# Performance work log

Hardware: AMD Instinct MI355X
Metric: run time of the kernel (lower is better)

The kernel has to match this reference:

```python
import jax, jax.numpy as jnp
import numpy as np
from jax import lax

V, E, H, T = 100000, 256, 256, 8192
FL, FN, NC = 5, 128, 20


def setup_inputs() -> dict:
    key = jax.random.key(0)
    ks = jax.random.split(key, 12)
    s = 0.05
    return {
        "docs": jax.random.randint(ks[0], (1, T), 0, V),
        "docs_length": jnp.array([T]),
        "labels": jax.random.randint(ks[1], (1,), 0, NC),
        "iteration": 0,
        "embed_W": jax.random.uniform(ks[2], (V, E), jnp.float32, -0.1, 0.1),
        "w_ih": jax.random.normal(ks[3], (4 * H, E), jnp.float32) * s,
        "w_hh": jax.random.normal(ks[4], (4 * H, H), jnp.float32) * s,
        "b_ih": jax.random.normal(ks[5], (4 * H,), jnp.float32) * s,
        "b_hh": jax.random.normal(ks[6], (4 * H,), jnp.float32) * s,
        "conv_w": jax.random.normal(ks[7], (FN, 1, FL, H), jnp.float32) * s,
        "conv_b": jax.random.normal(ks[8], (FN,), jnp.float32) * s,
        "logits_w": jax.random.uniform(ks[9], (NC, FN), jnp.float32, -0.1, 0.1),
        "logits_b": jnp.zeros((NC,), jnp.float32),
    }


def _forward(docs, labels, embed_W, w_ih, w_hh, b_ih, b_hh, conv_w, conv_b, logits_w, logits_b):
    # embed -> ReLU (dropout is identity at p=0)
    x = jax.nn.relu(embed_W[docs[0]])  # (T, E)

    b = b_ih + b_hh

    def step(carry, xt):
        h, c = carry
        g = xt @ w_ih.T + h @ w_hh.T + b  # (4H,)
        i, f, gg, o = jnp.split(g, 4)
        i = jax.nn.sigmoid(i)
        f = jax.nn.sigmoid(f)
        gg = jnp.tanh(gg)
        o = jax.nn.sigmoid(o)
        c = f * c + i * gg
        h = o * jnp.tanh(c)
        return (h, c), h

    init = (jnp.zeros((H,), x.dtype), jnp.zeros((H,), x.dtype))
    _, hs = lax.scan(step, init, x)  # (T, H)

    # Conv2d(1, FN, (FL, H)) valid: (1,1,T,H) -> (1,FN,T-FL+1,1)
    feat = lax.conv_general_dilated(
        hs[None, None, :, :], conv_w, window_strides=(1, 1), padding="VALID",
        dimension_numbers=("NCHW", "OIHW", "NCHW"))
    feat = feat[0, :, :, 0] + conv_b[:, None]  # (FN, T-FL+1)

    # AdaptiveMaxPool2d((FN,1)) == max over time
    pooled = jnp.max(feat, axis=1)  # (FN,)

    logits = pooled @ logits_w.T + logits_b  # (NC,)
    logp = jax.nn.log_softmax(logits)
    loss = -logp[labels[0]]
    acc = (jnp.argmax(logp) == labels[0]).astype(jnp.float32)
    return loss, acc


def reference(docs, docs_length, labels, iteration, embed_W, w_ih, w_hh, b_ih, b_hh,
              conv_w, conv_b, logits_w, logits_b):
    return _forward(docs, labels, embed_W, w_ih, w_hh, b_ih, b_hh,
                    conv_w, conv_b, logits_w, logits_b)
```

## Files before the change

### kernel.cpp

```cpp
#include <hip/hip_runtime.h>
#include <math.h>

#define T_LEN 8192

typedef float f32x4 __attribute__((ext_vector_type(4)));
typedef int   i32x8 __attribute__((ext_vector_type(8)));

#define DPP_MAX(x, ctrl) fmaxf((x), __int_as_float(__builtin_amdgcn_update_dpp(0, __float_as_int(x), (ctrl), 0xF, 0xF, true)))

__device__ __forceinline__ float fsig(float x) {
    x = fminf(30.f, fmaxf(-30.f, x));
    float e = __expf(-x);
    return __builtin_amdgcn_rcpf(1.f + e);
}
__device__ __forceinline__ float ftanh(float x) {
    x = fminf(15.f, fmaxf(-15.f, x));
    float e = __expf(-2.f * x);
    return (1.f - e) * __builtin_amdgcn_rcpf(1.f + e);
}

__device__ __forceinline__ unsigned char enc_e4m3(float x) {
#if __has_builtin(__builtin_amdgcn_cvt_pk_fp8_f32)
    int v = __builtin_amdgcn_cvt_pk_fp8_f32(x, 0.f, 0, false);
    return (unsigned char)(v & 0xff);
#else
    unsigned u = __float_as_uint(x);
    unsigned s = (u >> 24) & 0x80u;
    float a = fabsf(x);
    if (a > 448.f) a = 448.f;
    if (a < 9.765625e-4f) return (unsigned char)s;
    int e = ((int)((__float_as_uint(a) >> 23) & 0xffu)) - 127;
    int eu = e < -6 ? -6 : e;
    float ulp = exp2f((float)(eu - 3));
    float q = rintf(a / ulp);
    int mant, ee;
    if (eu == -6 && q < 8.f) { mant = (int)q; ee = 0; }
    else {
        if (q >= 16.f) { q *= 0.5f; eu += 1; }
        mant = (int)q - 8; ee = eu + 7;
        if (ee > 15 || (ee == 15 && mant > 6)) { ee = 15; mant = 6; }
    }
    return (unsigned char)(s | (unsigned)(ee << 3) | (unsigned)mant);
#endif
}
__device__ __forceinline__ unsigned pk4(float a, float b, float c, float d) {
    return (unsigned)enc_e4m3(a) | ((unsigned)enc_e4m3(b) << 8)
         | ((unsigned)enc_e4m3(c) << 16) | ((unsigned)enc_e4m3(d) << 24);
}

__device__ __forceinline__ unsigned enc_e2m3(float x) {
    unsigned s = (__float_as_uint(x) >> 31) << 5;
    float a = fabsf(x);
    a = fminf(a, 7.5f);
    if (a < 0.0625f) return s;
    int e = ((int)((__float_as_uint(a) >> 23) & 0xffu)) - 127;
    int eu = e < 0 ? 0 : e;
    float ulp = __int_as_float((unsigned)(eu + 124) << 23);
    float q = rintf(a * __builtin_amdgcn_rcpf(ulp));
    int E, M;
    if (e < 0) {
        if (q >= 8.f) { E = 1; M = 0; }
        else { E = 0; M = (int)q; }
    } else {
        if (q >= 16.f) { q = 8.f; eu += 1; }
        if (eu > 2) { E = 3; M = 7; }
        else { E = eu + 1; M = (int)q - 8; }
    }
    return s | (unsigned)(E << 3) | (unsigned)M;
}

__global__ __launch_bounds__(256) void pack_w6(
    const float* __restrict__ w_hh,
    unsigned* __restrict__ w6)
{
    int idx = blockIdx.x * 256 + threadIdx.x;
    int l  = idx & 63;
    int kt = (idx >> 6) & 1;
    int rt = (idx >> 7) & 7;
    int w  = idx >> 10;
    int rw = l & 15, kg = l >> 4;
    int rowp = ((8 * w + rt) << 4) + rw;
    int orow = ((rowp & 3) << 8) + (rowp >> 2);
    const float* s = w_hh + (size_t)orow * 256 + 128 * kt + 32 * kg;
    unsigned d[6] = {0, 0, 0, 0, 0, 0};
#pragma unroll
    for (int j = 0; j < 32; ++j) {
        unsigned c = enc_e2m3(s[j] * 32.f);
        int bit = 6 * j;
        d[bit >> 5] |= c << (bit & 31);
        if ((bit & 31) > 26) d[(bit >> 5) + 1] |= c >> (32 - (bit & 31));
    }
    unsigned* o = w6 + (size_t)idx * 8;
    o[0] = d[0]; o[1] = d[1]; o[2] = d[2];
    o[3] = d[3]; o[4] = d[4]; o[5] = d[5];
    o[6] = 0;    o[7] = 0;
}

__global__ __launch_bounds__(256, 4) void gemm_pre(
    const int* __restrict__ docs,
    const float* __restrict__ embW,
    const float* __restrict__ w_ih,
    const float* __restrict__ b_ih,
    const float* __restrict__ b_hh,
    float* __restrict__ pre)
{
    __shared__ __align__(16) float As[16][68];
    __shared__ __align__(16) float Bs[16][68];
    __shared__ int rowid[64];
    const int bt = blockIdx.x;
    const int bj = blockIdx.y;
    const int tid = threadIdx.x;
    if (tid < 64) rowid[tid] = docs[bt * 64 + tid];
    __syncthreads();
    const int ti = tid & 15, tj = tid >> 4;
    const int r = tid & 63;
    const int kk4 = (tid >> 6) * 4;
    float acc[4][4];
#pragma unroll
    for (int ii = 0; ii < 4; ++ii)
#pragma unroll
        for (int jj = 0; jj < 4; ++jj) acc[ii][jj] = 0.f;

    for (int k0 = 0; k0 < 256; k0 += 16) {
        float4 av = *(const float4*)(embW + (size_t)rowid[r] * 256 + k0 + kk4);
        float4 bv = *(const float4*)(w_ih + (size_t)(bj * 64 + r) * 256 + k0 + kk4);
        As[kk4 + 0][r] = fmaxf(av.x, 0.f);
        As[kk4 + 1][r] = fmaxf(av.y, 0.f);
        As[kk4 + 2][r] = fmaxf(av.z, 0.f);
        As[kk4 + 3][r] = fmaxf(av.w, 0.f);
        Bs[kk4 + 0][r] = bv.x;
        Bs[kk4 + 1][r] = bv.y;
        Bs[kk4 + 2][r] = bv.z;
        Bs[kk4 + 3][r] = bv.w;
        __syncthreads();
#pragma unroll
        for (int kk = 0; kk < 16; ++kk) {
            float4 a = *(const float4*)&As[kk][ti * 4];
            float4 b = *(const float4*)&Bs[kk][tj * 4];
            acc[0][0] += a.x * b.x; acc[0][1] += a.x * b.y; acc[0][2] += a.x * b.z; acc[0][3] += a.x * b.w;
            acc[1][0] += a.y * b.x; acc[1][1] += a.y * b.y; acc[1][2] += a.y * b.z; acc[1][3] += a.y * b.w;
            acc[2][0] += a.z * b.x; acc[2][1] += a.z * b.y; acc[2][2] += a.z * b.z; acc[2][3] += a.z * b.w;
            acc[3][0] += a.w * b.x; acc[3][1] += a.w * b.y; acc[3][2] += a.w * b.z; acc[3][3] += a.w * b.w;
        }
        __syncthreads();
    }
#pragma unroll
    for (int ii = 0; ii < 4; ++ii) {
        int t = bt * 64 + ti * 4 + ii;
#pragma unroll
        for (int jj = 0; jj < 4; ++jj) {
            int j = bj * 64 + tj * 4 + jj;
            int jp = ((j & 255) << 2) | (j >> 8);
            pre[(size_t)t * 1024 + jp] = acc[ii][jj] + b_ih[j] + b_hh[j];
        }
    }
}

__global__ __launch_bounds__(512, 2) void lstm_scan_mx6(
    const float* __restrict__ pre,
    const unsigned* __restrict__ w6,
    float* __restrict__ hs)
{
    const int tid = threadIdx.x;
    const int w  = tid >> 6;
    const int l  = tid & 63;
    const int rw = l & 15;
    const int kg = l >> 4;
    const float INV = 1.f / 128.f;

    __shared__ __align__(16) unsigned char h6pk[2][256];
    __shared__ __align__(16) float ldsPre[2][1024];

    i32x8 wA[8][2];
#pragma unroll
    for (int rt = 0; rt < 8; ++rt) {
#pragma unroll
        for (int kt = 0; kt < 2; ++kt) {
            const unsigned* s = w6 + (size_t)(((w * 8 + rt) * 2 + kt) * 64 + l) * 8;
            uint4 lo = *(const uint4*)s;
            uint2 hi = *(const uint2*)(s + 4);
            i32x8 v;
            v[0] = (int)lo.x; v[1] = (int)lo.y; v[2] = (int)lo.z;
            v[3] = (int)lo.w; v[4] = (int)hi.x; v[5] = (int)hi.y;
            v[6] = 0; v[7] = 0;
            wA[rt][kt] = v;
        }
    }

    for (int i = tid; i < 512; i += 512) h6pk[0][i] = 0;
    {
        float2 p = *(const float2*)(pre + 2 * tid);
        *(float2*)&ldsPre[0][2 * tid] = p;
    }

    const bool isup = (rw < 8);
    const int u = 32 * w + 4 * (rw & 7) + kg;
    float c_st = 0.f;

    const bool iswr = (rw < 8) && (kg < 3);
    const int bby = 8 * kg + rw;
    const int j0  = (4 * bby) / 3;
    const int rsh = 8 * bby - 6 * j0;
    const int lj0 = 16 * (j0 & 3) + (j0 >> 2);
    const int j1  = j0 + 1;
    const int lj1 = 16 * (j1 & 3) + (j1 >> 2);

    const float* pnext = pre + 1024 + 2 * tid;
    float* hsp = hs + u;
    __syncthreads();

    for (int t = 0; t < T_LEN; ++t) {
        const int PW = t & 1;
        const int PR = PW ^ 1;

        f32x4 p4 = *(const f32x4*)&ldsPre[PW][4 * u];

        float2 pv = *(const float2*)pnext;
        if (t + 2 < T_LEN) pnext += 1024;

        i32x8 bq[2];
#pragma unroll
        for (int kt = 0; kt < 2; ++kt) {
            const unsigned char* bp = &h6pk[PR][(4 * kt + kg) * 32];
            uint4 lo = *(const uint4*)bp;
            uint2 hi = *(const uint2*)(bp + 16);
            i32x8 b;
            b[0] = (int)lo.x; b[1] = (int)lo.y; b[2] = (int)lo.z; b[3] = (int)lo.w;
            b[4] = (int)hi.x; b[5] = (int)hi.y; b[6] = 0; b[7] = 0;
            bq[kt] = b;
        }

        f32x4 acc[8];
#pragma unroll
        for (int rt = 0; rt < 8; ++rt) acc[rt] = (f32x4){0.f, 0.f, 0.f, 0.f};
#pragma unroll
        for (int rt = 0; rt < 8; ++rt)
#pragma unroll
            for (int kt = 0; kt < 2; ++kt)
                acc[rt] = __builtin_amdgcn_mfma_scale_f32_16x16x128_f8f6f4(
                    wA[rt][kt], bq[kt], acc[rt],
                    2, 2,
                    0, 0x7f7f7f7f,
                    0, 0x7f7f7f7f);

        int code = 0;
        if (isup) {
            f32x4 av = acc[0];
            av = (rw == 1) ? acc[1] : av;
            av = (rw == 2) ? acc[2] : av;
            av = (rw == 3) ? acc[3] : av;
            av = (rw == 4) ? acc[4] : av;
            av = (rw == 5) ? acc[5] : av;
            av = (rw == 6) ? acc[6] : av;
            av = (rw == 7) ? acc[7] : av;
            float gi = fmaf(av.x, INV, p4.x);
            float gf = fmaf(av.y, INV, p4.y);
            float gg = fmaf(av.z, INV, p4.z);
            float go = fmaf(av.w, INV, p4.w);
            float si = fsig(gi);
            float sf = fsig(gf);
            float tg = ftanh(gg);
            float so = fsig(go);
            c_st = sf * c_st + si * tg;
            float h = so * ftanh(c_st);
            hsp[0] = h;
            code = (int)enc_e2m3(h * 4.f);
        }
        hsp += 256;

        int c0 = __shfl(code, lj0, 64);
        int c1 = __shfl(code, lj1, 64);
        if (iswr) {
            unsigned byte = (((unsigned)c0 >> rsh) | ((unsigned)c1 << (6 - rsh))) & 0xffu;
            h6pk[PW][w * 32 + bby] = (unsigned char)byte;
        }

        *(float2*)&ldsPre[PR][2 * tid] = pv;

        __syncthreads();
    }
}

__global__ __launch_bounds__(512, 2) void lstm_scan_mx8(
    const float* __restrict__ pre,
    const float* __restrict__ w_hh,
    float* __restrict__ hs)
{
    const int tid = threadIdx.x;
    const int w  = tid >> 6;
    const int l  = tid & 63;
    const int rw = l & 15;
    const int kg = l >> 4;
    const float INV = 1.f / 32768.f;

    __shared__ __align__(16) unsigned char h8[2 * 256];
    __shared__ __align__(16) float ldsPre[2][1024];

    i32x8 wA[8][2];
#pragma unroll
    for (int rt = 0; rt < 8; ++rt) {
#pragma unroll
        for (int kt = 0; kt < 2; ++kt) {
            int rowp = ((8 * w + rt) << 4) + rw;
            int orow = ((rowp & 3) << 8) + (rowp >> 2);
            const float* s = w_hh + (size_t)orow * 256 + 128 * kt + 32 * kg;
            i32x8 v;
#pragma unroll
            for (int d = 0; d < 8; ++d) {
                float4 f = *(const float4*)(s + 4 * d);
                v[d] = (int)pk4(f.x * 512.f, f.y * 512.f, f.z * 512.f, f.w * 512.f);
            }
            wA[rt][kt] = v;
        }
    }

    for (int i = tid; i < 512; i += 512) h8[i] = 0;
    {
        float2 p = *(const float2*)(pre + 2 * tid);
        *(float2*)&ldsPre[0][2 * tid] = p;
    }
    float c_st = 0.f;
    const bool isup = (rw < 8);
    const int u = 32 * w + 4 * (rw & 7) + kg;
    const float* pnext = pre + 1024 + 2 * tid;
    float* hsp = hs + u;
    __syncthreads();

    for (int t = 0; t < T_LEN; ++t) {
        const int PW = t & 1;
        const int PR = PW ^ 1;

        f32x4 p4 = *(const f32x4*)&ldsPre[PW][4 * u];

        float2 pv = *(const float2*)pnext;
        if (t + 2 < T_LEN) pnext += 1024;

        i32x8 bq[2];
#pragma unroll
        for (int kt = 0; kt < 2; ++kt) {
            const unsigned char* bp = &h8[PR * 256 + 128 * kt + 32 * kg];
            uint4 lo = *(const uint4*)bp;
            uint4 hi = *(const uint4*)(bp + 16);
            i32x8 b;
            b[0] = (int)lo.x; b[1] = (int)lo.y; b[2] = (int)lo.z; b[3] = (int)lo.w;
            b[4] = (int)hi.x; b[5] = (int)hi.y; b[6] = (int)hi.z; b[7] = (int)hi.w;
            bq[kt] = b;
        }

        f32x4 acc[8];
#pragma unroll
        for (int rt = 0; rt < 8; ++rt) acc[rt] = (f32x4){0.f, 0.f, 0.f, 0.f};
#pragma unroll
        for (int rt = 0; rt < 8; ++rt)
#pragma unroll
            for (int kt = 0; kt < 2; ++kt)
                acc[rt] = __builtin_amdgcn_mfma_scale_f32_16x16x128_f8f6f4(
                    wA[rt][kt], bq[kt], acc[rt],
                    0, 0,
                    0, 0x7f7f7f7f,
                    0, 0x7f7f7f7f);

        if (isup) {
            f32x4 av = acc[0];
            av = (rw == 1) ? acc[1] : av;
            av = (rw == 2) ? acc[2] : av;
            av = (rw == 3) ? acc[3] : av;
            av = (rw == 4) ? acc[4] : av;
            av = (rw == 5) ? acc[5] : av;
            av = (rw == 6) ? acc[6] : av;
            av = (rw == 7) ? acc[7] : av;
            float gi = fmaf(av.x, INV, p4.x);
            float gf = fmaf(av.y, INV, p4.y);
            float gg = fmaf(av.z, INV, p4.z);
            float go = fmaf(av.w, INV, p4.w);
            float si = fsig(gi);
            float sf = fsig(gf);
            float tg = ftanh(gg);
            float so = fsig(go);
            c_st = sf * c_st + si * tg;
            float h = so * ftanh(c_st);
            hsp[0] = h;
            h8[PW * 256 + u] = enc_e4m3(h * 64.f);
        }
        hsp += 256;

        *(float2*)&ldsPre[PR][2 * tid] = pv;

        __syncthreads();
    }
}

__global__ __launch_bounds__(256) void conv_pool(
    const float* __restrict__ hs,
    const float* __restrict__ cw,
    const float* __restrict__ cb,
    float* __restrict__ part)
{
    __shared__ __align__(16) float hst[68 * 260];
    __shared__ __align__(16) float cwS[128 * 68];
    const int blk = blockIdx.x;
    const int t0 = blk * 64;
    const int tid = threadIdx.x;
    const int i = tid & 15;
    const int g = tid >> 4;

    for (int e = tid; e < 68 * 64; e += 256) {
        int rr = e >> 6;
        int c4 = (e & 63) * 4;
        int tg = t0 + rr; if (tg > 8191) tg = 8191;
        float4 v = *(const float4*)(hs + (size_t)tg * 256 + c4);
        *(float4*)&hst[rr * 260 + c4] = v;
    }

    float acc[4][8];
#pragma unroll
    for (int tt = 0; tt < 4; ++tt)
#pragma unroll
        for (int j = 0; j < 8; ++j) acc[tt][j] = 0.f;

    for (int l = 0; l < 5; ++l) {
        for (int hc = 0; hc < 4; ++hc) {
            __syncthreads();
            {
                int n = tid >> 1;
                int hb = (tid & 1) * 32;
                const float* src = cw + (size_t)n * 1280 + l * 256 + hc * 64 + hb;
                float* dst = &cwS[n * 68 + hb];
#pragma unroll
                for (int q = 0; q < 8; ++q) {
                    float4 v = *(const float4*)(src + 4 * q);
                    *(float4*)(dst + 4 * q) = v;
                }
            }
            __syncthreads();
#pragma unroll 4
            for (int q = 0; q < 16; ++q) {
                float4 hvv[4];
#pragma unroll
                for (int tt = 0; tt < 4; ++tt)
                    hvv[tt] = *(const float4*)&hst[(i + 16 * tt + l) * 260 + hc * 64 + 4 * q];
#pragma unroll
                for (int j = 0; j < 8; ++j) {
                    float4 wv = *(const float4*)&cwS[(g + 16 * j) * 68 + 4 * q];
#pragma unroll
                    for (int tt = 0; tt < 4; ++tt) {
                        acc[tt][j] += hvv[tt].x * wv.x + hvv[tt].y * wv.y
                                    + hvv[tt].z * wv.z + hvv[tt].w * wv.w;
                    }
                }
            }
        }
    }

    float m[8];
#pragma unroll
    for (int j = 0; j < 8; ++j) {
        int n = g + 16 * j;
        float cbn = cb[n];
        float mm = -INFINITY;
#pragma unroll
        for (int tt = 0; tt < 4; ++tt) {
            int t = t0 + i + 16 * tt;
            float v = acc[tt][j] + cbn;
            if (t < 8188) mm = fmaxf(mm, v);
        }
        mm = DPP_MAX(mm, 0xB1);
        mm = DPP_MAX(mm, 0x4E);
        mm = DPP_MAX(mm, 0x141);
        mm = DPP_MAX(mm, 0x140);
        m[j] = mm;
    }
    if (i == 0) {
#pragma unroll
        for (int j = 0; j < 8; ++j)
            part[(size_t)blk * 128 + g + 16 * j] = m[j];
    }
}

__global__ void final_head(
    const float* __restrict__ part,
    const float* __restrict__ logits_w,
    const float* __restrict__ logits_b,
    const int* __restrict__ labels,
    float* __restrict__ out)
{
    __shared__ float pooled[128];
    __shared__ float lgt[20];
    int tid = threadIdx.x;
    float mx = -INFINITY;
    for (int b = 0; b < 128; ++b) mx = fmaxf(mx, part[(size_t)b * 128 + tid]);
    pooled[tid] = mx;
    __syncthreads();
    if (tid < 20) {
        float s = logits_b[tid];
        for (int k = 0; k < 128; ++k) s += logits_w[tid * 128 + k] * pooled[k];
        lgt[tid] = s;
    }
    __syncthreads();
    if (tid == 0) {
        float m = lgt[0]; int am = 0;
        for (int c2 = 1; c2 < 20; ++c2) { if (lgt[c2] > m) { m = lgt[c2]; am = c2; } }
        float se = 0.f;
        for (int c2 = 0; c2 < 20; ++c2) se += expf(lgt[c2] - m);
        float lse = m + logf(se);
        int lbl = labels[0];
        out[0] = -(lgt[lbl] - lse);
        out[1] = (am == lbl) ? 1.f : 0.f;
    }
}

extern "C" void kernel_launch(void* const* d_in, const int* in_sizes, int n_in,
                              void* d_out, int out_size, void* d_ws, size_t ws_size,
                              hipStream_t stream) {
    (void)in_sizes; (void)n_in; (void)out_size;
    const int*   docs   = (const int*)d_in[0];
    const int*   labels = (const int*)d_in[2];
    const float* embW   = (const float*)d_in[4];
    const float* w_ih   = (const float*)d_in[5];
    const float* w_hh   = (const float*)d_in[6];
    const float* b_ih   = (const float*)d_in[7];
    const float* b_hh   = (const float*)d_in[8];
    const float* cw     = (const float*)d_in[9];
    const float* cb     = (const float*)d_in[10];
    const float* lw     = (const float*)d_in[11];
    const float* lb     = (const float*)d_in[12];
    float* out = (float*)d_out;

    char* ws = (char*)d_ws;
    float*    pre  = (float*)(ws);
    float*    hs   = (float*)(ws + 33554432);
    float*    part = (float*)(ws + 41943040);
    unsigned* w6   = (unsigned*)(ws + 42008576);

    hipFuncAttributes a6;
    bool ok6 = (hipFuncGetAttributes(&a6, (const void*)lstm_scan_mx6) == hipSuccess)
               && (a6.localSizeBytes == 0)
               && (ws_size >= (size_t)42270720);

    gemm_pre<<<dim3(128, 16, 1), 256, 0, stream>>>(docs, embW, w_ih, b_ih, b_hh, pre);
    if (ok6) {
        pack_w6<<<32, 256, 0, stream>>>(w_hh, w6);
        lstm_scan_mx6<<<1, 512, 0, stream>>>(pre, w6, hs);
    } else {
        lstm_scan_mx8<<<1, 512, 0, stream>>>(pre, w_hh, hs);
    }
    conv_pool<<<128, 256, 0, stream>>>(hs, cw, cb, part);
    final_head<<<1, 128, 0, stream>>>(part, lw, lb, labels, out);
}
```

Baseline: 6.155 ms.

## Add 4-wave LSTM scan kernel with 16 MFMA tiles per wave

Adds a 256-thread, 4-wave variant of the single-block LSTM recurrence. Each wave holds 16 row tiles of the FP6-packed recurrent weights in registers, so every lane computes one hidden unit with no idle half-waves. It also prefetches the next timestep's gate preactivations a step ahead instead of staging them through LDS, and computes tanh via an unclamped sigmoid. The goal is to cut per-step barrier and sync cost and the number of waves on the serial critical path, at the price of more MFMAs per wave and higher register pressure. Dropping the clamp risks inf/NaN for extreme inputs, and the kernel falls back to the 8-wave path if it spills.

```diff
diff --git a/kernel.cpp b/kernel.cpp
--- a/kernel.cpp
+++ b/kernel.cpp
@@ -9,11 +9,15 @@
 #define DPP_MAX(x, ctrl) fmaxf((x), __int_as_float(__builtin_amdgcn_update_dpp(0, __float_as_int(x), (ctrl), 0xF, 0xF, true)))
 
 __device__ __forceinline__ float fsig(float x) {
+    float e = __expf(-x);
+    return __builtin_amdgcn_rcpf(1.f + e);
+}
+__device__ __forceinline__ float fsig_c(float x) {
     x = fminf(30.f, fmaxf(-30.f, x));
     float e = __expf(-x);
     return __builtin_amdgcn_rcpf(1.f + e);
 }
-__device__ __forceinline__ float ftanh(float x) {
+__device__ __forceinline__ float ftanh_c(float x) {
     x = fminf(15.f, fmaxf(-15.f, x));
     float e = __expf(-2.f * x);
     return (1.f - e) * __builtin_amdgcn_rcpf(1.f + e);
@@ -76,10 +80,9 @@
     int idx = blockIdx.x * 256 + threadIdx.x;
     int l  = idx & 63;
     int kt = (idx >> 6) & 1;
-    int rt = (idx >> 7) & 7;
-    int w  = idx >> 10;
+    int gt = idx >> 7;
     int rw = l & 15, kg = l >> 4;
-    int rowp = ((8 * w + rt) << 4) + rw;
+    int rowp = (gt << 4) + rw;
     int orow = ((rowp & 3) << 8) + (rowp >> 2);
     const float* s = w_hh + (size_t)orow * 256 + 128 * kt + 32 * kg;
     unsigned d[6] = {0, 0, 0, 0, 0, 0};
@@ -156,6 +159,121 @@
     }
 }
 
+__global__ __launch_bounds__(256, 1) void lstm_scan_mx6w4(
+    const float* __restrict__ pre,
+    const unsigned* __restrict__ w6,
+    float* __restrict__ hs)
+{
+    const int tid = threadIdx.x;
+    const int w  = tid >> 6;
+    const int l  = tid & 63;
+    const int rto = l & 15;
+    const int kg  = l >> 4;
+    const float INV = 1.f / 128.f;
+
+    __shared__ __align__(16) unsigned char h6pk[2][256];
+
+    i32x8 wA[16][2];
+#pragma unroll
+    for (int rtt = 0; rtt < 16; ++rtt) {
+#pragma unroll
+        for (int kt = 0; kt < 2; ++kt) {
+            int gt = 16 * w + rtt;
+            const unsigned* s = w6 + (size_t)((gt * 2 + kt) * 64 + l) * 8;
+            uint4 lo = *(const uint4*)s;
+            uint2 hi = *(const uint2*)(s + 4);
+            i32x8 v;
+            v[0] = (int)lo.x; v[1] = (int)lo.y; v[2] = (int)lo.z;
+            v[3] = (int)lo.w; v[4] = (int)hi.x; v[5] = (int)hi.y;
+            v[6] = 0; v[7] = 0;
+            wA[rtt][kt] = v;
+        }
+    }
+
+    for (int i = tid; i < 512; i += 256) ((unsigned char*)h6pk)[i] = 0;
+
+    const int u = 64 * w + 4 * rto + kg;
+    float c_st = 0.f;
+
+    const bool iswr = (l < 48);
+    const int s_  = (l >= 24) ? 1 : 0;
+    const int b_  = l - 24 * s_;
+    const int j0  = (4 * b_) / 3;
+    const int rsh = 8 * b_ - 6 * j0;
+    const int j1  = j0 + 1;
+    const int lj0 = 16 * (j0 & 3) + 8 * s_ + (j0 >> 2);
+    const int lj1 = 16 * (j1 & 3) + 8 * s_ + (j1 >> 2);
+    const int wofs = (2 * w + s_) * 32 + b_;
+
+    f32x4 p4c = *(const f32x4*)(pre + 4 * u);
+    const float* pp = pre + 1024 + 4 * u;
+    float* hsp = hs + u;
+    __syncthreads();
+
+    for (int t = 0; t < T_LEN; ++t) {
+        const int PW = t & 1;
+        const int PR = PW ^ 1;
+
+        f32x4 p4n = *(const f32x4*)pp;
+        if (t + 2 < T_LEN) pp += 1024;
+
+        i32x8 bq0, bq1;
+        {
+            const unsigned char* bp0 = &h6pk[PR][kg * 32];
+            uint4 lo = *(const uint4*)bp0;
+            uint2 hi = *(const uint2*)(bp0 + 16);
+            bq0[0] = (int)lo.x; bq0[1] = (int)lo.y; bq0[2] = (int)lo.z;
+            bq0[3] = (int)lo.w; bq0[4] = (int)hi.x; bq0[5] = (int)hi.y;
+            bq0[6] = 0; bq0[7] = 0;
+            const unsigned char* bp1 = &h6pk[PR][(4 + kg) * 32];
+            uint4 lo1 = *(const uint4*)bp1;
+            uint2 hi1 = *(const uint2*)(bp1 + 16);
+            bq1[0] = (int)lo1.x; bq1[1] = (int)lo1.y; bq1[2] = (int)lo1.z;
+            bq1[3] = (int)lo1.w; bq1[4] = (int)hi1.x; bq1[5] = (int)hi1.y;
+            bq1[6] = 0; bq1[7] = 0;
+        }
+
+        f32x4 acc[16];
+#pragma unroll
+        for (int rtt = 0; rtt < 16; ++rtt) {
+            acc[rtt] = __builtin_amdgcn_mfma_scale_f32_16x16x128_f8f6f4(
+                wA[rtt][0], bq0, (f32x4){0.f, 0.f, 0.f, 0.f},
+                2, 2, 0, 0x7f7f7f7f, 0, 0x7f7f7f7f);
+            acc[rtt] = __builtin_amdgcn_mfma_scale_f32_16x16x128_f8f6f4(
+                wA[rtt][1], bq1, acc[rtt],
+                2, 2, 0, 0x7f7f7f7f, 0, 0x7f7f7f7f);
+        }
+
+        f32x4 av = acc[0];
+#pragma unroll
+        for (int k = 1; k < 16; ++k) av = (rto == k) ? acc[k] : av;
+
+        float gi = fmaf(av.x, INV, p4c.x);
+        float gf = fmaf(av.y, INV, p4c.y);
+        float gg = fmaf(av.z, INV, p4c.z);
+        float go = fmaf(av.w, INV, p4c.w);
+        float si = fsig(gi);
+        float sf = fsig(gf);
+        float tg = 2.f * fsig(2.f * gg) - 1.f;
+        float so = fsig(go);
+        c_st = sf * c_st + si * tg;
+        float h = so * (2.f * fsig(2.f * c_st) - 1.f);
+        hsp[0] = h;
+        hsp += 256;
+        int code = (int)enc_e2m3(h * 4.f);
+
+        int c0 = __shfl(code, lj0, 64);
+        int c1 = __shfl(code, lj1, 64);
+        if (iswr) {
+            unsigned byte = (((unsigned)c0 >> rsh) | ((unsigned)c1 << (6 - rsh))) & 0xffu;
+            h6pk[PW][wofs] = (unsigned char)byte;
+        }
+
+        p4c = p4n;
+        __syncthreads();
+    }
+}
+
 __global__ __launch_bounds__(512, 2) void lstm_scan_mx6(
     const float* __restrict__ pre,
     const unsigned* __restrict__ w6,
@@ -239,9 +357,7 @@
             for (int kt = 0; kt < 2; ++kt)
                 acc[rt] = __builtin_amdgcn_mfma_scale_f32_16x16x128_f8f6f4(
                     wA[rt][kt], bq[kt], acc[rt],
-                    2, 2,
-                    0, 0x7f7f7f7f,
-                    0, 0x7f7f7f7f);
+                    2, 2, 0, 0x7f7f7f7f, 0, 0x7f7f7f7f);
 
         int code = 0;
         if (isup) {
@@ -257,12 +373,12 @@
             float gf = fmaf(av.y, INV, p4.y);
             float gg = fmaf(av.z, INV, p4.z);
             float go = fmaf(av.w, INV, p4.w);
-            float si = fsig(gi);
-            float sf = fsig(gf);
-            float tg = ftanh(gg);
-            float so = fsig(go);
+            float si = fsig_c(gi);
+            float sf = fsig_c(gf);
+            float tg = ftanh_c(gg);
+            float so = fsig_c(go);
             c_st = sf * c_st + si * tg;
-            float h = so * ftanh(c_st);
+            float h = so * ftanh_c(c_st);
             hsp[0] = h;
             code = (int)enc_e2m3(h * 4.f);
         }
@@ -356,9 +472,7 @@
             for (int kt = 0; kt < 2; ++kt)
                 acc[rt] = __builtin_amdgcn_mfma_scale_f32_16x16x128_f8f6f4(
                     wA[rt][kt], bq[kt], acc[rt],
-                    0, 0,
-                    0, 0x7f7f7f7f,
-                    0, 0x7f7f7f7f);
+                    0, 0, 0, 0x7f7f7f7f, 0, 0x7f7f7f7f);
 
         if (isup) {
             f32x4 av = acc[0];
@@ -373,12 +487,12 @@
             float gf = fmaf(av.y, INV, p4.y);
             float gg = fmaf(av.z, INV, p4.z);
             float go = fmaf(av.w, INV, p4.w);
-            float si = fsig(gi);
-            float sf = fsig(gf);
-            float tg = ftanh(gg);
-            float so = fsig(go);
+            float si = fsig_c(gi);
+            float sf = fsig_c(gf);
+            float tg = ftanh_c(gg);
+            float so = fsig_c(go);
             c_st = sf * c_st + si * tg;
-            float h = so * ftanh(c_st);
+            float h = so * ftanh_c(c_st);
             hsp[0] = h;
             h8[PW * 256 + u] = enc_e4m3(h * 64.f);
         }
@@ -532,15 +646,20 @@
     float*    part = (float*)(ws + 41943040);
     unsigned* w6   = (unsigned*)(ws + 42008576);
 
-    hipFuncAttributes a6;
-    bool ok6 = (hipFuncGetAttributes(&a6, (const void*)lstm_scan_mx6) == hipSuccess)
-               && (a6.localSizeBytes == 0)
-               && (ws_size >= (size_t)42270720);
+    bool ws_ok = (ws_size >= (size_t)42270720);
+    hipFuncAttributes a4, a6;
+    bool ok4 = ws_ok
+        && (hipFuncGetAttributes(&a4, (const void*)lstm_scan_mx6w4) == hipSuccess)
+        && (a4.localSizeBytes == 0);
+    bool ok6 = ws_ok
+        && (hipFuncGetAttributes(&a6, (const void*)lstm_scan_mx6) == hipSuccess)
+        && (a6.localSizeBytes == 0);
 
     gemm_pre<<<dim3(128, 16, 1), 256, 0, stream>>>(docs, embW, w_ih, b_ih, b_hh, pre);
-    if (ok6) {
+    if (ok4 || ok6) {
         pack_w6<<<32, 256, 0, stream>>>(w_hh, w6);
-        lstm_scan_mx6<<<1, 512, 0, stream>>>(pre, w6, hs);
+        if (ok4) lstm_scan_mx6w4<<<1, 256, 0, stream>>>(pre, w6, hs);
+        else     lstm_scan_mx6<<<1, 512, 0, stream>>>(pre, w6, hs);
     } else {
         lstm_scan_mx8<<<1, 512, 0, stream>>>(pre, w_hh, hs);
     }
```

Result: no change. 6.209 ms (+0.9%).
